# Performance work log

Measured on AMD Instinct MI355X. Metric: run time of the kernel, lower is better.

The kernel has to match this reference:

```python
import jax, jax.numpy as jnp
import numpy as np

N_NODES = 100000
N_EDGES = 1200000
IN_DIM = 256
HID = 64


def _spmm(rows, cols, vals, M):
    # sparse (COO) @ dense: gather source rows, scale by edge vals, scatter-add to dest
    gathered = M[cols] * vals[:, None]          # [E, d]
    return jax.ops.segment_sum(gathered, rows, num_segments=N_NODES)


def _gcn_embed(rows, cols, vals, X, W1, b1, W2, b2):
    # layer 1: SELU(A @ (X W1) + b1)
    Z = _spmm(rows, cols, vals, X @ W1) + b1
    Z = jax.nn.selu(Z)
    # layer 2: A @ (Z W2) + b2 (no activation)
    Z = _spmm(rows, cols, vals, Z @ W2) + b2
    # row-wise L2 normalize (F.normalize, p=2, dim=1)
    norm = jnp.sqrt(jnp.sum(Z * Z, axis=1, keepdims=True))
    return Z / jnp.maximum(norm, 1e-12)


def setup_inputs() -> dict:
    key = jax.random.key(0)
    ks = jax.random.split(key, 10)
    X1 = jax.random.normal(ks[0], (N_NODES, IN_DIM), dtype=jnp.float32)
    X2 = jax.random.normal(ks[1], (N_NODES, IN_DIM), dtype=jnp.float32)
    rows1 = jax.random.randint(ks[2], (N_EDGES,), 0, N_NODES, dtype=jnp.int32)
    cols1 = jax.random.randint(ks[3], (N_EDGES,), 0, N_NODES, dtype=jnp.int32)
    vals1 = jax.random.uniform(ks[4], (N_EDGES,), dtype=jnp.float32)
    rows2 = jax.random.randint(ks[5], (N_EDGES,), 0, N_NODES, dtype=jnp.int32)
    cols2 = jax.random.randint(ks[6], (N_EDGES,), 0, N_NODES, dtype=jnp.int32)
    vals2 = jax.random.uniform(ks[7], (N_EDGES,), dtype=jnp.float32)
    # Xavier-uniform weights, zero biases (reset_parameters)
    lim1 = float(np.sqrt(6.0 / (IN_DIM + HID)))
    lim2 = float(np.sqrt(6.0 / (HID + HID)))
    W1 = jax.random.uniform(ks[8], (IN_DIM, HID), dtype=jnp.float32, minval=-lim1, maxval=lim1)
    W2 = jax.random.uniform(ks[9], (HID, HID), dtype=jnp.float32, minval=-lim2, maxval=lim2)
    b1 = jnp.zeros((HID,), dtype=jnp.float32)
    b2 = jnp.zeros((HID,), dtype=jnp.float32)
    return {"X1": X1, "X2": X2, "rows1": rows1, "cols1": cols1, "vals1": vals1,
            "rows2": rows2, "cols2": cols2, "vals2": vals2,
            "W1": W1, "b1": b1, "W2": W2, "b2": b2}


def reference(X1, X2, rows1, cols1, vals1, rows2, cols2, vals2, W1, b1, W2, b2):
    Z1 = _gcn_embed(rows1, cols1, vals1, X1, W1, b1, W2, b2)
    Z2 = _gcn_embed(rows2, cols2, vals2, X2, W1, b1, W2, b2)
    return (Z1, Z2)
```

## Files before the change

kernel.cpp:

```cpp
#include <hip/hip_runtime.h>
#include <hip/hip_bf16.h>


#define RPB 512
#define EPB 4096
#define MAXB 8192

typedef __attribute__((ext_vector_type(8))) short short8;
typedef __attribute__((ext_vector_type(4))) short short4v;
typedef __attribute__((ext_vector_type(4))) float f32x4;

__device__ __forceinline__ float selu_f(float x) {
    const float scale = 1.0507009873554805f;
    const float alpha = 1.6732632423543772f;
    return x > 0.0f ? scale * x : scale * alpha * (__expf(x) - 1.0f);
}

__device__ __forceinline__ short f2bf(float x) {
    unsigned u = __float_as_uint(x);
    u += 0x7FFF + ((u >> 16) & 1);
    return (short)(u >> 16);
}
__device__ __forceinline__ float bf2f(short h) {
    return __uint_as_float(((unsigned)(unsigned short)h) << 16);
}

__global__ void scan_a(const int* __restrict__ counts, int* __restrict__ offs,
                       int* __restrict__ partials, int N) {
    __shared__ int sh[256];
    int tid = threadIdx.x;
    int base = blockIdx.x * 1024 + tid * 4;
    int4 c = make_int4(0, 0, 0, 0);
    if (base + 3 < N) {
        c = *(const int4*)(counts + base);
    } else {
        if (base + 0 < N) c.x = counts[base + 0];
        if (base + 1 < N) c.y = counts[base + 1];
        if (base + 2 < N) c.z = counts[base + 2];
        if (base + 3 < N) c.w = counts[base + 3];
    }
    int tsum = c.x + c.y + c.z + c.w;
    sh[tid] = tsum;
    __syncthreads();
    int val = tsum;
    for (int d = 1; d < 256; d <<= 1) {
        int t = (tid >= d) ? sh[tid - d] : 0;
        __syncthreads();
        val += t;
        sh[tid] = val;
        __syncthreads();
    }
    int excl = val - tsum;
    int4 o;
    o.x = excl; o.y = o.x + c.x; o.z = o.y + c.y; o.w = o.z + c.z;
    if (base + 3 < N) {
        *(int4*)(offs + base) = o;
    } else {
        if (base + 0 < N) offs[base + 0] = o.x;
        if (base + 1 < N) offs[base + 1] = o.y;
        if (base + 2 < N) offs[base + 2] = o.z;
        if (base + 3 < N) offs[base + 3] = o.w;
    }
    if (tid == 255) partials[blockIdx.x] = val;
}

__global__ void scan_b(int* __restrict__ partials, int nb) {
    __shared__ int sh[128];
    int tid = threadIdx.x;
    int v = (tid < nb) ? partials[tid] : 0;
    sh[tid] = v;
    __syncthreads();
    int val = v;
    for (int d = 1; d < 128; d <<= 1) {
        int t = (tid >= d) ? sh[tid - d] : 0;
        __syncthreads();
        val += t;
        sh[tid] = val;
        __syncthreads();
    }
    if (tid < nb) partials[tid] = val - v;
}

__global__ void scan_c(int* __restrict__ offs, const int* __restrict__ partials,
                       int N, int E) {
    int tid = threadIdx.x;
    int base = blockIdx.x * 1024 + tid * 4;
    int add = partials[blockIdx.x];
    if (base + 3 < N) {
        int4 o = *(int4*)(offs + base);
        o.x += add; o.y += add; o.z += add; o.w += add;
        *(int4*)(offs + base) = o;
    } else {
        for (int t = 0; t < 4; t++)
            if (base + t < N) offs[base + t] += add;
    }
    if (blockIdx.x == 0 && tid == 0) offs[N] = E;
}

__global__ __launch_bounds__(256) void bucket_hist(const int* __restrict__ rows,
                                                   int* __restrict__ cntT,
                                                   int E, int nbA, int NB) {
    __shared__ int cnt[256];
    int tid = threadIdx.x;
    cnt[tid] = 0;
    __syncthreads();
    int e0 = blockIdx.x * EPB;
#pragma unroll
    for (int k = 0; k < EPB / 256; k++) {
        int e = e0 + k * 256 + tid;
        if (e < E) atomicAdd(&cnt[rows[e] >> 9], 1);
    }
    __syncthreads();
    if (tid < NB) cntT[tid * nbA + blockIdx.x] = cnt[tid];
}

__global__ __launch_bounds__(256) void coarse_scatter(const int* __restrict__ rows,
                                                      const int* __restrict__ cols,
                                                      const float* __restrict__ vals,
                                                      const int* __restrict__ csOffs,
                                                      int2* __restrict__ ecvA,
                                                      int E, int nbA, int NB) {
    __shared__ int cnt[256];
    __shared__ int loc[256];
    __shared__ int gof[256];
    __shared__ int dstBase[EPB];
    __shared__ int2 eLDS[EPB];
    int tid = threadIdx.x, blk = blockIdx.x;
    int e0 = blk * EPB;
    cnt[tid] = 0;
    __syncthreads();
#pragma unroll
    for (int k = 0; k < EPB / 256; k++) {
        int e = e0 + k * 256 + tid;
        if (e < E) atomicAdd(&cnt[rows[e] >> 9], 1);
    }
    __syncthreads();
    int my = cnt[tid];
    loc[tid] = my;
    __syncthreads();
    int val = my;
    for (int d = 1; d < 256; d <<= 1) {
        int t = (tid >= d) ? loc[tid - d] : 0;
        __syncthreads();
        val += t;
        loc[tid] = val;
        __syncthreads();
    }
    int excl = val - my;
    loc[tid] = excl;
    cnt[tid] = excl;
    gof[tid] = (tid < NB) ? csOffs[tid * nbA + blk] : 0;
    __syncthreads();
#pragma unroll
    for (int k = 0; k < EPB / 256; k++) {
        int e = e0 + k * 256 + tid;
        if (e < E) {
            int r = rows[e];
            int b = r >> 9;
            int p = atomicAdd(&cnt[b], 1);
            eLDS[p] = make_int2(((r & (RPB - 1)) << 17) | cols[e],
                                __float_as_int(vals[e]));
            dstBase[p] = gof[b] - loc[b];
        }
    }
    __syncthreads();
    int nE = min(EPB, E - e0);
    for (int j = tid; j < nE; j += 256)
        ecvA[dstBase[j] + j] = eLDS[j];
}

__global__ __launch_bounds__(256) void fine_sort(const int* __restrict__ csOffs,
                                                 const int2* __restrict__ ecvA,
                                                 int2* __restrict__ ecv,
                                                 int* __restrict__ offs,
                                                 int nbA, int N, int E) {
    __shared__ int rcnt[RPB], roff[RPB], rcur[RPB];
    __shared__ int sh[256];
    __shared__ int2 eLDS[MAXB];
    int b = blockIdx.x, tid = threadIdx.x;
    int bs = csOffs[b * nbA];
    int be = csOffs[(b + 1) * nbA];
    int cntE = be - bs;
    if (cntE > MAXB) cntE = MAXB;
    rcnt[tid] = 0;
    rcnt[tid + 256] = 0;
    __syncthreads();
    for (int j = tid; j < cntE; j += 256)
        atomicAdd(&rcnt[ecvA[bs + j].x >> 17], 1);
    __syncthreads();
    int a0 = rcnt[2 * tid], a1 = rcnt[2 * tid + 1];
    int ps = a0 + a1;
    sh[tid] = ps;
    __syncthreads();
    int val = ps;
    for (int d = 1; d < 256; d <<= 1) {
        int t = (tid >= d) ? sh[tid - d] : 0;
        __syncthreads();
        val += t;
        sh[tid] = val;
        __syncthreads();
    }
    int exclPair = val - ps;
    roff[2 * tid] = exclPair;
    roff[2 * tid + 1] = exclPair + a0;
    rcur[2 * tid] = exclPair;
    rcur[2 * tid + 1] = exclPair + a0;
    __syncthreads();
    int row0 = b * RPB;
    for (int t2 = tid; t2 < RPB; t2 += 256) {
        int row = row0 + t2;
        if (row <= N) offs[row] = bs + roff[t2];
    }
    if (b == 0 && tid == 0) offs[N] = E;
    for (int j = tid; j < cntE; j += 256) {
        int2 p = ecvA[bs + j];
        int pos = atomicAdd(&rcur[p.x >> 17], 1);
        if (pos < MAXB) eLDS[pos] = make_int2(p.x & 0x1FFFF, p.y);
    }
    __syncthreads();
    for (int j = tid; j < cntE; j += 256)
        ecv[bs + j] = eLDS[j];
}

__global__ void prep_w(const float* __restrict__ W, short* __restrict__ th,
                       short* __restrict__ tl, int K) {
    int idx = blockIdx.x * 256 + threadIdx.x;
    if (idx < K * 64) {
        int k = idx >> 6, n = idx & 63;
        float x = W[idx];
        short h = f2bf(x);
        short l = f2bf(x - bf2f(h));
        th[n * K + k] = h;
        tl[n * K + k] = l;
    }
}

__global__ __launch_bounds__(256) void gemm_mfma(const float* __restrict__ A,
                                                 const short* __restrict__ Wth,
                                                 const short* __restrict__ Wtl,
                                                 float* __restrict__ C, int M, int K) {
    __shared__ short Ah[64 * 72], Al[64 * 72];
    __shared__ short Wh[64 * 72], Wl[64 * 72];
    int tid = threadIdx.x;
    int wave = tid >> 6, lane = tid & 63;
    int m = lane & 15, q = lane >> 4;
    int row0 = blockIdx.x * 64;
    f32x4 acc[4] = {{0.f, 0.f, 0.f, 0.f}, {0.f, 0.f, 0.f, 0.f},
                    {0.f, 0.f, 0.f, 0.f}, {0.f, 0.f, 0.f, 0.f}};
    for (int kc = 0; kc < K; kc += 64) {
#pragma unroll
        for (int v = 0; v < 4; v++) {
            int idx = v * 256 + tid;
            int i = idx >> 4;
            int j4 = (idx & 15) * 4;
            int gr = row0 + i;
            float4 g = make_float4(0.f, 0.f, 0.f, 0.f);
            if (gr < M) g = *(const float4*)(A + (size_t)gr * K + kc + j4);
            short4v h, l;
            h.x = f2bf(g.x); l.x = f2bf(g.x - bf2f(h.x));
            h.y = f2bf(g.y); l.y = f2bf(g.y - bf2f(h.y));
            h.z = f2bf(g.z); l.z = f2bf(g.z - bf2f(h.z));
            h.w = f2bf(g.w); l.w = f2bf(g.w - bf2f(h.w));
            *(short4v*)(&Ah[i * 72 + j4]) = h;
            *(short4v*)(&Al[i * 72 + j4]) = l;
        }
#pragma unroll
        for (int v = 0; v < 4; v++) {
            int idx = v * 256 + tid;
            int n = idx >> 4;
            int k4 = (idx & 15) * 4;
            short4v hv = *(const short4v*)(Wth + (size_t)n * K + kc + k4);
            short4v lv = *(const short4v*)(Wtl + (size_t)n * K + kc + k4);
            *(short4v*)(&Wh[n * 72 + k4]) = hv;
            *(short4v*)(&Wl[n * 72 + k4]) = lv;
        }
        __syncthreads();
        int ar = (16 * wave + m) * 72;
        short8 ah0 = *(const short8*)(&Ah[ar + q * 8]);
        short8 ah1 = *(const short8*)(&Ah[ar + 32 + q * 8]);
        short8 al0 = *(const short8*)(&Al[ar + q * 8]);
        short8 al1 = *(const short8*)(&Al[ar + 32 + q * 8]);
#pragma unroll
        for (int nt = 0; nt < 4; nt++) {
            int nb = (nt * 16 + m) * 72;
            short8 bh0 = *(const short8*)(&Wh[nb + q * 8]);
            short8 bh1 = *(const short8*)(&Wh[nb + 32 + q * 8]);
            short8 bl0 = *(const short8*)(&Wl[nb + q * 8]);
            short8 bl1 = *(const short8*)(&Wl[nb + 32 + q * 8]);
            acc[nt] = __builtin_amdgcn_mfma_f32_16x16x32_bf16(ah0, bh0, acc[nt], 0, 0, 0);
            acc[nt] = __builtin_amdgcn_mfma_f32_16x16x32_bf16(al0, bh0, acc[nt], 0, 0, 0);
            acc[nt] = __builtin_amdgcn_mfma_f32_16x16x32_bf16(ah0, bl0, acc[nt], 0, 0, 0);
            acc[nt] = __builtin_amdgcn_mfma_f32_16x16x32_bf16(ah1, bh1, acc[nt], 0, 0, 0);
            acc[nt] = __builtin_amdgcn_mfma_f32_16x16x32_bf16(al1, bh1, acc[nt], 0, 0, 0);
            acc[nt] = __builtin_amdgcn_mfma_f32_16x16x32_bf16(ah1, bl1, acc[nt], 0, 0, 0);
        }
        __syncthreads();
    }
#pragma unroll
    for (int nt = 0; nt < 4; nt++) {
#pragma unroll
        for (int r = 0; r < 4; r++) {
            int grow = row0 + 16 * wave + q * 4 + r;
            if (grow < M) C[(size_t)grow * 64 + nt * 16 + m] = acc[nt][r];
        }
    }
}

__device__ __forceinline__ void spmm_row4(const int* __restrict__ offs,
                                          const int2* __restrict__ ecv,
                                          const float* __restrict__ H,
                                          int row, int g, int f4,
                                          float& ax, float& ay, float& az, float& aw) {
    int s = offs[row], e = offs[row + 1];
    s = __builtin_amdgcn_readfirstlane(s);
    e = __builtin_amdgcn_readfirstlane(e);
    ax = ay = az = aw = 0.f;
    for (int i = s; i < e; i += 8) {
        int i0 = i + g, i1 = i + 4 + g;
        int2 p0 = ecv[i0 < e ? i0 : (e - 1)];
        int2 p1 = ecv[i1 < e ? i1 : (e - 1)];
        float v0 = (i0 < e) ? __int_as_float(p0.y) : 0.f;
        float v1 = (i1 < e) ? __int_as_float(p1.y) : 0.f;
        float4 h0 = *(const float4*)(H + (size_t)p0.x * 64 + f4);
        float4 h1 = *(const float4*)(H + (size_t)p1.x * 64 + f4);
        ax = fmaf(v0, h0.x, ax); ay = fmaf(v0, h0.y, ay);
        az = fmaf(v0, h0.z, az); aw = fmaf(v0, h0.w, aw);
        ax = fmaf(v1, h1.x, ax); ay = fmaf(v1, h1.y, ay);
        az = fmaf(v1, h1.z, az); aw = fmaf(v1, h1.w, aw);
    }
#pragma unroll
    for (int d = 16; d <= 32; d <<= 1) {
        ax += __shfl_xor(ax, d, 64);
        ay += __shfl_xor(ay, d, 64);
        az += __shfl_xor(az, d, 64);
        aw += __shfl_xor(aw, d, 64);
    }
}

__global__ __launch_bounds__(256) void spmm_selu(const int* __restrict__ offs,
                                                 const int2* __restrict__ ecv,
                                                 const float* __restrict__ H,
                                                 const float* __restrict__ bias,
                                                 float* __restrict__ out, int N) {
    int row = blockIdx.x * 4 + (threadIdx.x >> 6);
    if (row >= N) return;
    int lane = threadIdx.x & 63;
    int g = lane >> 4, f4 = (lane & 15) * 4;
    float ax, ay, az, aw;
    spmm_row4(offs, ecv, H, row, g, f4, ax, ay, az, aw);
    float4 b = *(const float4*)(bias + f4);
    if (g == 0) {
        float4 o;
        o.x = selu_f(ax + b.x);
        o.y = selu_f(ay + b.y);
        o.z = selu_f(az + b.z);
        o.w = selu_f(aw + b.w);
        *(float4*)(out + (size_t)row * 64 + f4) = o;
    }
}

__global__ __launch_bounds__(256) void spmm_norm(const int* __restrict__ offs,
                                                 const int2* __restrict__ ecv,
                                                 const float* __restrict__ H,
                                                 const float* __restrict__ bias,
                                                 float* __restrict__ out, int N) {
    int row = blockIdx.x * 4 + (threadIdx.x >> 6);
    if (row >= N) return;
    int lane = threadIdx.x & 63;
    int g = lane >> 4, f4 = (lane & 15) * 4;
    float ax, ay, az, aw;
    spmm_row4(offs, ecv, H, row, g, f4, ax, ay, az, aw);
    float4 b = *(const float4*)(bias + f4);
    float zx = ax + b.x, zy = ay + b.y, zz = az + b.z, zw = aw + b.w;
    float s2 = zx * zx + zy * zy + zz * zz + zw * zw;
#pragma unroll
    for (int d = 1; d <= 8; d <<= 1) s2 += __shfl_xor(s2, d, 64);
    float inv = 1.0f / fmaxf(sqrtf(s2), 1e-12f);
    if (g == 0) {
        float4 o;
        o.x = zx * inv; o.y = zy * inv; o.z = zz * inv; o.w = zw * inv;
        *(float4*)(out + (size_t)row * 64 + f4) = o;
    }
}

extern "C" void kernel_launch(void* const* d_in, const int* in_sizes, int n_in,
                              void* d_out, int out_size, void* d_ws, size_t ws_size,
                              hipStream_t stream) {
    const int IN_DIM = 256, HID = 64;
    const int N = in_sizes[0] / IN_DIM;
    const int E = in_sizes[2];

    const float* X[2]    = {(const float*)d_in[0], (const float*)d_in[1]};
    const int*   rows[2] = {(const int*)d_in[2], (const int*)d_in[5]};
    const int*   cols[2] = {(const int*)d_in[3], (const int*)d_in[6]};
    const float* vals[2] = {(const float*)d_in[4], (const float*)d_in[7]};
    const float* W1 = (const float*)d_in[8];
    const float* b1 = (const float*)d_in[9];
    const float* W2 = (const float*)d_in[10];
    const float* b2 = (const float*)d_in[11];
    float* out = (float*)d_out;

    const int NB  = (N + RPB - 1) / RPB;
    const int nbA = (E + EPB - 1) / EPB;
    const int M   = NB * nbA;
    const int nbScanM = (M + 1023) / 1024;
    const int nbGemm = (N + 63) / 64;
    const int nbRow  = (N + 3) / 4;

    auto align16 = [](char* p) { return (char*)(((uintptr_t)p + 15) & ~(uintptr_t)15); };
    char* w = (char*)d_ws;
    float* bufA   = (float*)w; w += (size_t)N * HID * sizeof(float);
    float* bufB   = (float*)w; w += (size_t)N * HID * sizeof(float);
    w = align16(w);
    int2*  ecv    = (int2*)w;  w += (size_t)E * sizeof(int2);
    w = align16(w);
    int*   cntT   = (int*)w;   w += (size_t)M * sizeof(int);
    w = align16(w);
    int*   csOffs = (int*)w;   w += (size_t)(M + 1) * sizeof(int);
    w = align16(w);
    int*   offs   = (int*)w;   w += (size_t)(N + 1) * sizeof(int);
    w = align16(w);
    int*   partials = (int*)w; w += 1024;
    w = align16(w);
    short* w1th = (short*)w;   w += (size_t)64 * IN_DIM * sizeof(short);
    short* w1tl = (short*)w;   w += (size_t)64 * IN_DIM * sizeof(short);
    short* w2th = (short*)w;   w += (size_t)64 * HID * sizeof(short);
    short* w2tl = (short*)w;   w += (size_t)64 * HID * sizeof(short);
    int2*  ecvA = (int2*)bufA;

    prep_w<<<(IN_DIM * 64 + 255) / 256, 256, 0, stream>>>(W1, w1th, w1tl, IN_DIM);
    prep_w<<<(HID * 64 + 255) / 256, 256, 0, stream>>>(W2, w2th, w2tl, HID);

    for (int g = 0; g < 2; g++) {
        bucket_hist<<<nbA, 256, 0, stream>>>(rows[g], cntT, E, nbA, NB);
        scan_a<<<nbScanM, 256, 0, stream>>>(cntT, csOffs, partials, M);
        scan_b<<<1, 128, 0, stream>>>(partials, nbScanM);
        scan_c<<<nbScanM, 256, 0, stream>>>(csOffs, partials, M, E);
        coarse_scatter<<<nbA, 256, 0, stream>>>(rows[g], cols[g], vals[g], csOffs,
                                                ecvA, E, nbA, NB);
        fine_sort<<<NB, 256, 0, stream>>>(csOffs, ecvA, ecv, offs, nbA, N, E);
        gemm_mfma<<<nbGemm, 256, 0, stream>>>(X[g], w1th, w1tl, bufA, N, IN_DIM);
        spmm_selu<<<nbRow, 256, 0, stream>>>(offs, ecv, bufA, b1, bufB, N);
        gemm_mfma<<<nbGemm, 256, 0, stream>>>(bufB, w2th, w2tl, bufA, N, HID);
        spmm_norm<<<nbRow, 256, 0, stream>>>(offs, ecv, bufA, b2,
                                             out + (size_t)g * N * HID, N);
    }
}
```

Baseline: 616.1 us.

## Rewrite dense GEMM to keep W resident in LDS and A fragments in registers

Replaces the tiled split-bf16 MFMA GEMM with a persistent-style kernel. The whole transposed W (hi and lo parts) is loaded once per block into XOR-swizzled LDS. Each wave then loops over 16-row tiles, loading its A fragments straight from global memory into registers, which removes the per-K-chunk LDS staging and the __syncthreads barriers. The first GEMM uses a fixed grid of 512 blocks of 512 threads, which raises register pressure (KS=8 short8 arrays) and makes occupancy depend on the launch bounds.

After: 792.9 us. +28.7%, slower.

```diff
diff --git a/kernel.cpp b/kernel.cpp
--- a/kernel.cpp
+++ b/kernel.cpp
@@ -235,73 +235,75 @@
     }
 }
 
-__global__ __launch_bounds__(256) void gemm_mfma(const float* __restrict__ A,
-                                                 const short* __restrict__ Wth,
-                                                 const short* __restrict__ Wtl,
-                                                 float* __restrict__ C, int M, int K) {
-    __shared__ short Ah[64 * 72], Al[64 * 72];
-    __shared__ short Wh[64 * 72], Wl[64 * 72];
+template<int K>
+__global__ __launch_bounds__(512, 4) void gemm_reg(const float* __restrict__ A,
+                                                   const short* __restrict__ Wth,
+                                                   const short* __restrict__ Wtl,
+                                                   float* __restrict__ C, int M) {
+    constexpr int KS = K / 32;
+    __shared__ short Wh[64 * K];
+    __shared__ short Wl[64 * K];
     int tid = threadIdx.x;
+    {
+        int n = tid >> 3;
+        int xm = (n & 7) << 3;
+#pragma unroll
+        for (int i = 0; i < K / 64; i++) {
+            int k0 = ((tid & 7) + 8 * i) * 8;
+            int src = n * K + k0;
+            int dst = n * K + (k0 ^ xm);
+            *(short8*)(&Wh[dst]) = *(const short8*)(Wth + src);
+            *(short8*)(&Wl[dst]) = *(const short8*)(Wtl + src);
+        }
+    }
+    __syncthreads();
     int wave = tid >> 6, lane = tid & 63;
     int m = lane & 15, q = lane >> 4;
-    int row0 = blockIdx.x * 64;
-    f32x4 acc[4] = {{0.f, 0.f, 0.f, 0.f}, {0.f, 0.f, 0.f, 0.f},
-                    {0.f, 0.f, 0.f, 0.f}, {0.f, 0.f, 0.f, 0.f}};
-    for (int kc = 0; kc < K; kc += 64) {
-#pragma unroll
-        for (int v = 0; v < 4; v++) {
-            int idx = v * 256 + tid;
-            int i = idx >> 4;
-            int j4 = (idx & 15) * 4;
-            int gr = row0 + i;
-            float4 g = make_float4(0.f, 0.f, 0.f, 0.f);
-            if (gr < M) g = *(const float4*)(A + (size_t)gr * K + kc + j4);
-            short4v h, l;
-            h.x = f2bf(g.x); l.x = f2bf(g.x - bf2f(h.x));
-            h.y = f2bf(g.y); l.y = f2bf(g.y - bf2f(h.y));
-            h.z = f2bf(g.z); l.z = f2bf(g.z - bf2f(h.z));
-            h.w = f2bf(g.w); l.w = f2bf(g.w - bf2f(h.w));
-            *(short4v*)(&Ah[i * 72 + j4]) = h;
-            *(short4v*)(&Al[i * 72 + j4]) = l;
+    int nT = (M + 15) >> 4;
+    int gw = gridDim.x * 8;
+    for (int t = blockIdx.x * 8 + wave; t < nT; t += gw) {
+        int arow = t * 16 + m;
+        if (arow >= M) arow = M - 1;
+        const float* a = A + (size_t)arow * K + q * 8;
+        short8 ah[KS], al[KS];
+#pragma unroll
+        for (int ks = 0; ks < KS; ks++) {
+            float4 f0 = *(const float4*)(a + ks * 32);
+            float4 f1 = *(const float4*)(a + ks * 32 + 4);
+            float f[8] = {f0.x, f0.y, f0.z, f0.w, f1.x, f1.y, f1.z, f1.w};
+            short8 h, l;
+#pragma unroll
+            for (int j = 0; j < 8; j++) {
+                short hh = f2bf(f[j]);
+                h[j] = hh;
+                l[j] = f2bf(f[j] - bf2f(hh));
+            }
+            ah[ks] = h; al[ks] = l;
         }
-#pragma unroll
-        for (int v = 0; v < 4; v++) {
-            int idx = v * 256 + tid;
-            int n = idx >> 4;
-            int k4 = (idx & 15) * 4;
-            short4v hv = *(const short4v*)(Wth + (size_t)n * K + kc + k4);
-            short4v lv = *(const short4v*)(Wtl + (size_t)n * K + kc + k4);
-            *(short4v*)(&Wh[n * 72 + k4]) = hv;
-            *(short4v*)(&Wl[n * 72 + k4]) = lv;
+        f32x4 acc[4] = {{0.f, 0.f, 0.f, 0.f}, {0.f, 0.f, 0.f, 0.f},
+                        {0.f, 0.f, 0.f, 0.f}, {0.f, 0.f, 0.f, 0.f}};
+#pragma unroll
+        for (int nt = 0; nt < 4; nt++) {
+            int n = nt * 16 + m;
+            int base = n * K;
+            int xm = (n & 7) << 3;
+#pragma unroll
+            for (int ks = 0; ks < KS; ks++) {
+                int off = base + ((ks * 32 + q * 8) ^ xm);
+                short8 bh = *(const short8*)(&Wh[off]);
+                short8 bl = *(const short8*)(&Wl[off]);
+                acc[nt] = __builtin_amdgcn_mfma_f32_16x16x32_bf16(ah[ks], bh, acc[nt], 0, 0, 0);
+                acc[nt] = __builtin_amdgcn_mfma_f32_16x16x32_bf16(al[ks], bh, acc[nt], 0, 0, 0);
+                acc[nt] = __builtin_amdgcn_mfma_f32_16x16x32_bf16(ah[ks], bl, acc[nt], 0, 0, 0);
+            }
         }
-        __syncthreads();
-        int ar = (16 * wave + m) * 72;
-        short8 ah0 = *(const short8*)(&Ah[ar + q * 8]);
-        short8 ah1 = *(const short8*)(&Ah[ar + 32 + q * 8]);
-        short8 al0 = *(const short8*)(&Al[ar + q * 8]);
-        short8 al1 = *(const short8*)(&Al[ar + 32 + q * 8]);
 #pragma unroll
         for (int nt = 0; nt < 4; nt++) {
-            int nb = (nt * 16 + m) * 72;
-            short8 bh0 = *(const short8*)(&Wh[nb + q * 8]);
-            short8 bh1 = *(const short8*)(&Wh[nb + 32 + q * 8]);
-            short8 bl0 = *(const short8*)(&Wl[nb + q * 8]);
-            short8 bl1 = *(const short8*)(&Wl[nb + 32 + q * 8]);
-            acc[nt] = __builtin_amdgcn_mfma_f32_16x16x32_bf16(ah0, bh0, acc[nt], 0, 0, 0);
-            acc[nt] = __builtin_amdgcn_mfma_f32_16x16x32_bf16(al0, bh0, acc[nt], 0, 0, 0);
-            acc[nt] = __builtin_amdgcn_mfma_f32_16x16x32_bf16(ah0, bl0, acc[nt], 0, 0, 0);
-            acc[nt] = __builtin_amdgcn_mfma_f32_16x16x32_bf16(ah1, bh1, acc[nt], 0, 0, 0);
-            acc[nt] = __builtin_amdgcn_mfma_f32_16x16x32_bf16(al1, bh1, acc[nt], 0, 0, 0);
-            acc[nt] = __builtin_amdgcn_mfma_f32_16x16x32_bf16(ah1, bl1, acc[nt], 0, 0, 0);
-        }
-        __syncthreads();
-    }
-#pragma unroll
-    for (int nt = 0; nt < 4; nt++) {
-#pragma unroll
-        for (int r = 0; r < 4; r++) {
-            int grow = row0 + 16 * wave + q * 4 + r;
-            if (grow < M) C[(size_t)grow * 64 + nt * 16 + m] = acc[nt][r];
+#pragma unroll
+            for (int r = 0; r < 4; r++) {
+                int grow = t * 16 + q * 4 + r;
+                if (grow < M) C[(size_t)grow * 64 + nt * 16 + m] = acc[nt][r];
+            }
         }
     }
 }
@@ -404,8 +406,10 @@
     const int nbA = (E + EPB - 1) / EPB;
     const int M   = NB * nbA;
     const int nbScanM = (M + 1023) / 1024;
-    const int nbGemm = (N + 63) / 64;
     const int nbRow  = (N + 3) / 4;
+    const int nT = (N + 15) / 16;
+    const int nbG1 = 512;
+    const int nbG2 = (nT + 7) / 8;
 
     auto align16 = [](char* p) { return (char*)(((uintptr_t)p + 15) & ~(uintptr_t)15); };
     char* w = (char*)d_ws;
@@ -439,9 +443,9 @@
         coarse_scatter<<<nbA, 256, 0, stream>>>(rows[g], cols[g], vals[g], csOffs,
                                                 ecvA, E, nbA, NB);
         fine_sort<<<NB, 256, 0, stream>>>(csOffs, ecvA, ecv, offs, nbA, N, E);
-        gemm_mfma<<<nbGemm, 256, 0, stream>>>(X[g], w1th, w1tl, bufA, N, IN_DIM);
+        gemm_reg<256><<<nbG1, 512, 0, stream>>>(X[g], w1th, w1tl, bufA, N);
         spmm_selu<<<nbRow, 256, 0, stream>>>(offs, ecv, bufA, b1, bufB, N);
-        gemm_mfma<<<nbGemm, 256, 0, stream>>>(bufB, w2th, w2tl, bufA, N, HID);
+        gemm_reg<64><<<nbG2, 512, 0, stream>>>(bufB, w2th, w2tl, bufA, N);
         spmm_norm<<<nbRow, 256, 0, stream>>>(offs, ecv, bufA, b2,
                                              out + (size_t)g * N * HID, N);
     }
```
